# Kernel optimization log

Measured on AMD Instinct MI355X. Metric: run time of the kernel, lower is better.

The kernel has to match this reference:

```python
import jax, jax.numpy as jnp
import numpy as np

N_NODES = 50000
N_EDGES = 800000
DIMX = 64
DIMY = 32
NSMAT = 64
N_MID = 6  # six hidden nsmat->nsmat layers between the input and output projections


def setup_inputs() -> dict:
    key = jax.random.key(0)
    ks = jax.random.split(key, 10)
    node_features = jax.random.normal(ks[0], (N_NODES, DIMX), dtype=jnp.float32)
    edge_index = jax.random.randint(ks[1], (2, N_EDGES), 0, N_NODES, dtype=jnp.int64)
    s_in = 1.0 / np.sqrt(DIMX)
    s_mid = 1.0 / np.sqrt(NSMAT)
    w_in = jax.random.uniform(ks[2], (DIMX, NSMAT), jnp.float32, -s_in, s_in)
    b_in = jax.random.uniform(ks[3], (NSMAT,), jnp.float32, -s_in, s_in)
    w_mid = jax.random.uniform(ks[4], (N_MID, NSMAT, NSMAT), jnp.float32, -s_mid, s_mid)
    b_mid = jax.random.uniform(ks[5], (N_MID, NSMAT), jnp.float32, -s_mid, s_mid)
    w_out = jax.random.uniform(ks[6], (NSMAT, DIMY * DIMX), jnp.float32, -s_mid, s_mid)
    b_out = jax.random.uniform(ks[7], (DIMY * DIMX,), jnp.float32, -s_mid, s_mid)
    return {"node_features": node_features, "edge_index": edge_index,
            "w_in": w_in, "b_in": b_in, "w_mid": w_mid, "b_mid": b_mid,
            "w_out": w_out, "b_out": b_out}


def reference(node_features, edge_index, w_in, b_in, w_mid, b_mid, w_out, b_out):
    # per-node MLP producing a [dimy, dimx] sheaf matrix
    h = jax.nn.relu(node_features @ w_in + b_in)
    for i in range(N_MID):  # fixed small layer count
        h = jax.nn.relu(h @ w_mid[i] + b_mid[i])
    smat = (h @ w_out + b_out).reshape(-1, DIMY, DIMX)  # [N, dimy, dimx]
    # batched matrix-vector transform: q_n = smat_n @ x_n
    q = jnp.einsum('nyx,nx->ny', smat, node_features)  # [N, dimy]
    # LightGCN conv: out_i = sum_{(j->i) in E} q_j / sqrt(deg_j * deg_i)
    row, col = edge_index[0], edge_index[1]
    deg = jax.ops.segment_sum(jnp.ones((N_EDGES,), q.dtype), col, num_segments=N_NODES)
    dinv = jnp.where(deg > 0, jax.lax.rsqrt(jnp.maximum(deg, 1.0)), 0.0)
    norm = dinv[row] * dinv[col]  # [E]
    out = jax.ops.segment_sum(norm[:, None] * q[row], col, num_segments=N_NODES)
    return out
```

## Files before the change

kernel.cpp:

```cpp
#include <hip/hip_runtime.h>
#include <cstddef>

#define N_NODES_C 50000
#define N_NODES_PAD 50048
#define N_EDGES_C 800000
#define CAP 64

typedef _Float16 f16x8 __attribute__((ext_vector_type(8)));
typedef float    f32x4 __attribute__((ext_vector_type(4)));

constexpr int XSTR = 72;
constexpr int MQ_BLOCKS   = 782;
constexpr int DEG_BLOCKS  = 782;
constexpr int FILL_BLOCKS = 782;
constexpr int SCALE_BLOCKS = 391;

__device__ __forceinline__ void gll16(const void* g, void* l) {
    __builtin_amdgcn_global_load_lds(
        (const __attribute__((address_space(1))) void*)g,
        (__attribute__((address_space(3))) void*)l, 16, 0, 0);
}

__global__ void prep_w_kernel(const float* __restrict__ w_in,
                              const float* __restrict__ w_mid,
                              const float* __restrict__ w_out,
                              _Float16* __restrict__ wT,
                              _Float16* __restrict__ W3T)
{
    const int idx = blockIdx.x * 256 + threadIdx.x;
    if (idx < 7 * 4096) {
        const int l = idx >> 12, rem = idx & 4095;
        const int k = rem >> 6, j = rem & 63;
        const float v = (l == 0) ? w_in[k * 64 + j]
                                 : w_mid[(size_t)(l - 1) * 4096 + k * 64 + j];
        wT[(size_t)l * 4096 + j * 64 + k] = (_Float16)v;
    } else {
        const int i2 = idx - 7 * 4096;
        const int k = i2 >> 11, r = i2 & 2047;
        const int c = k >> 3;
        const int pos = ((c ^ (r & 7)) << 3) | (k & 7);
        W3T[(size_t)r * 64 + pos] = (_Float16)w_out[(size_t)k * 2048 + r];
    }
}

__launch_bounds__(256, 4)
__global__ void mega_kernel(const float* __restrict__ xf,
                            const float* __restrict__ b_in,
                            const float* __restrict__ b_mid,
                            const _Float16* __restrict__ wT,
                            const _Float16* __restrict__ W3T,
                            const float* __restrict__ b_out,
                            float* __restrict__ qs,
                            const int* __restrict__ col,
                            int* __restrict__ deg,
                            unsigned char* __restrict__ rank8)
{
    __shared__ _Float16 smem[16896];

    if (blockIdx.x >= MQ_BLOCKS) {
        const int base = (blockIdx.x - MQ_BLOCKS) * 1024 + threadIdx.x;
        #pragma unroll
        for (int u = 0; u < 4; ++u) {
            const int e = base + u * 256;
            if (e < N_EDGES_C)
                rank8[e] = (unsigned char)atomicAdd(&deg[col[e]], 1);
        }
        return;
    }

    const int t    = threadIdx.x;
    const int w    = t >> 6;
    const int lane = t & 63;
    const int quad = lane >> 4;
    const int lrow = lane & 15;
    const int node0 = blockIdx.x * 64 + w * 16;
    _Float16* hb = &smem[w * 16 * XSTR];

    {
        const int n = min(node0 + lrow, N_NODES_C - 1);
        const float4* src4 = (const float4*)(xf + (size_t)n * 64 + quad * 16);
        _Float16 tmp[16];
        #pragma unroll
        for (int i = 0; i < 4; ++i) {
            const float4 v = src4[i];
            tmp[i * 4 + 0] = (_Float16)v.x;
            tmp[i * 4 + 1] = (_Float16)v.y;
            tmp[i * 4 + 2] = (_Float16)v.z;
            tmp[i * 4 + 3] = (_Float16)v.w;
        }
        *(f16x8*)&hb[lrow * XSTR + quad * 16]     = *(f16x8*)&tmp[0];
        *(f16x8*)&hb[lrow * XSTR + quad * 16 + 8] = *(f16x8*)&tmp[8];
    }

    {
        const _Float16* wTl = wT;
        const float* bsrc = b_in;
        for (int l = 0; l < 7; ++l) {
            const f16x8 A0 = *(const f16x8*)&hb[lrow * XSTR + quad * 8];
            const f16x8 A1 = *(const f16x8*)&hb[lrow * XSTR + 32 + quad * 8];
            #pragma unroll
            for (int Nt = 0; Nt < 4; ++Nt) {
                const f16x8 B0 = *(const f16x8*)(wTl + (Nt * 16 + lrow) * 64 + quad * 8);
                const f16x8 B1 = *(const f16x8*)(wTl + (Nt * 16 + lrow) * 64 + 32 + quad * 8);
                const float bias = bsrc[Nt * 16 + lrow];
                f32x4 C = {0.f, 0.f, 0.f, 0.f};
                C = __builtin_amdgcn_mfma_f32_16x16x32_f16(A0, B0, C, 0, 0, 0);
                C = __builtin_amdgcn_mfma_f32_16x16x32_f16(A1, B1, C, 0, 0, 0);
                #pragma unroll
                for (int r = 0; r < 4; ++r) {
                    const float v = fmaxf(C[r] + bias, 0.f);
                    hb[(quad * 4 + r) * XSTR + Nt * 16 + lrow] = (_Float16)v;
                }
            }
            wTl += 4096;
            bsrc = b_mid + (size_t)l * 64;
        }
    }

    const int ra = node0 + lrow;
    const int na = min(ra, N_NODES_C - 1);

    f16x8 Bha[2];
    #pragma unroll
    for (int ks = 0; ks < 2; ++ks)
        Bha[ks] = *(const f16x8*)&hb[lrow * XSTR + ks * 32 + quad * 8];
    float4 xca[4];
    #pragma unroll
    for (int xt = 0; xt < 4; ++xt)
        xca[xt] = *(const float4*)(xf + (size_t)na * 64 + xt * 16 + quad * 4);

    __syncthreads();

    {
        float* lb = (float*)smem;
        const float* gb = b_out + (size_t)(w * 64 + lane) * 4;
        gll16(gb,        lb + w * 256);
        gll16(gb + 1024, lb + 1024 + w * 256);
        #pragma unroll
        for (int s = 0; s < 2; ++s) {
            _Float16* ld = &smem[4608 + s * 4096 + w * 512];
            const _Float16* gs = W3T + (size_t)s * 4096 + (size_t)(w * 64 + lane) * 8;
            gll16(gs,        ld);
            gll16(gs + 2048, ld + 2048);
        }
    }

    const int swz = lrow & 7;
    const int cp0 = ((quad)     ^ swz) * 8;
    const int cp1 = ((4 + quad) ^ swz) * 8;
    const float* lbf = (const float*)smem;

    int rcur = 0;
    for (int y = 0; y < 32; ++y) {
        if (y == 0)      asm volatile("s_waitcnt vmcnt(2)" ::: "memory");
        else if (y == 1) asm volatile("s_waitcnt vmcnt(3)" ::: "memory");
        else             asm volatile("s_waitcnt vmcnt(4)" ::: "memory");
        __builtin_amdgcn_s_barrier();
        __builtin_amdgcn_sched_barrier(0);

        {
            const int ys = (y + 2) & 31;
            const int ri = (rcur == 0) ? 2 : rcur - 1;
            _Float16* ld = &smem[4608 + ri * 4096 + w * 512];
            const _Float16* gs = W3T + (size_t)ys * 4096 + (size_t)(w * 64 + lane) * 8;
            gll16(gs,        ld);
            gll16(gs + 2048, ld + 2048);
        }

        const _Float16* cur = &smem[4608 + rcur * 4096];
        float qa = 0.f;
        #pragma unroll
        for (int xt = 0; xt < 4; ++xt) {
            const _Float16* rp = cur + (xt * 16 + lrow) * 64;
            const f16x8 A0 = *(const f16x8*)(rp + cp0);
            const f16x8 A1 = *(const f16x8*)(rp + cp1);
            f32x4 Ca = {0.f, 0.f, 0.f, 0.f};
            Ca = __builtin_amdgcn_mfma_f32_16x16x32_f16(A0, Bha[0], Ca, 0, 0, 0);
            Ca = __builtin_amdgcn_mfma_f32_16x16x32_f16(A1, Bha[1], Ca, 0, 0, 0);

            const float4 bf = *(const float4*)(lbf + y * 64 + xt * 16 + quad * 4);
            qa += (Ca[0] + bf.x) * xca[xt].x + (Ca[1] + bf.y) * xca[xt].y
                + (Ca[2] + bf.z) * xca[xt].z + (Ca[3] + bf.w) * xca[xt].w;
        }
        qa += __shfl_xor(qa, 16);
        qa += __shfl_xor(qa, 32);

        if (quad == (y >> 3)) {
            qs[(size_t)ra * 32 + y] = qa;
        }

        rcur = (rcur == 2) ? 0 : rcur + 1;
    }
}

__global__ void fill_scale_kernel(const int* __restrict__ row,
                                  const int* __restrict__ col,
                                  const unsigned char* __restrict__ rank8,
                                  const int* __restrict__ deg,
                                  float* __restrict__ qs,
                                  unsigned short* __restrict__ src16)
{
    if (blockIdx.x < FILL_BLOCKS) {
        const int base = blockIdx.x * 1024 + threadIdx.x;
        #pragma unroll
        for (int u = 0; u < 4; ++u) {
            const int e = base + u * 256;
            if (e < N_EDGES_C) {
                const int c = col[e];
                const int r = rank8[e];
                src16[(size_t)c * CAP + r] = (unsigned short)row[e];
            }
        }
    } else {
        const int sb = blockIdx.x - FILL_BLOCKS;
        #pragma unroll
        for (int k = 0; k < 4; ++k) {
            const int idx4 = k * (SCALE_BLOCKS * 256) + sb * 256 + threadIdx.x;
            const int rown = idx4 >> 3;
            const int d = (rown < N_NODES_C) ? deg[rown] : 0;
            const float dv = (d > 0) ? rsqrtf((float)d) : 0.f;
            float4* p = (float4*)qs + idx4;
            float4 v = *p;
            v.x *= dv; v.y *= dv; v.z *= dv; v.w *= dv;
            *p = v;
        }
    }
}

__global__ void gather_kernel(const int* __restrict__ deg,
                              const unsigned short* __restrict__ src16,
                              const float* __restrict__ qs,
                              float* __restrict__ out)
{
    const int t = threadIdx.x;
    const int node = blockIdx.x * 32 + (t >> 3);
    if (node >= N_NODES_C) return;
    const int yq = (t & 7) * 4;
    const int d = deg[node];
    const unsigned short* sp = src16 + (size_t)node * CAP;
    float4 acc = {0.f, 0.f, 0.f, 0.f};
    int s = 0;
    for (; s + 4 <= d; s += 4) {
        const ushort4 r4 = *(const ushort4*)(sp + s);
        const float4 a0 = *(const float4*)(qs + (size_t)r4.x * 32 + yq);
        const float4 a1 = *(const float4*)(qs + (size_t)r4.y * 32 + yq);
        const float4 a2 = *(const float4*)(qs + (size_t)r4.z * 32 + yq);
        const float4 a3 = *(const float4*)(qs + (size_t)r4.w * 32 + yq);
        acc.x += a0.x + a1.x + a2.x + a3.x;
        acc.y += a0.y + a1.y + a2.y + a3.y;
        acc.z += a0.z + a1.z + a2.z + a3.z;
        acc.w += a0.w + a1.w + a2.w + a3.w;
    }
    for (; s < d; ++s) {
        const float4 a = *(const float4*)(qs + (size_t)sp[s] * 32 + yq);
        acc.x += a.x; acc.y += a.y; acc.z += a.z; acc.w += a.w;
    }
    const float dv = (d > 0) ? rsqrtf((float)d) : 0.f;
    float4 r;
    r.x = acc.x * dv; r.y = acc.y * dv; r.z = acc.z * dv; r.w = acc.w * dv;
    *(float4*)(out + (size_t)node * 32 + yq) = r;
}

extern "C" void kernel_launch(void* const* d_in, const int* in_sizes, int n_in,
                              void* d_out, int out_size, void* d_ws, size_t ws_size,
                              hipStream_t stream)
{
    const float* xf    = (const float*)d_in[0];
    const int*   eidx  = (const int*)d_in[1];
    const float* w_in  = (const float*)d_in[2];
    const float* b_in  = (const float*)d_in[3];
    const float* w_mid = (const float*)d_in[4];
    const float* b_mid = (const float*)d_in[5];
    const float* w_out = (const float*)d_in[6];
    const float* b_out = (const float*)d_in[7];
    float* out = (float*)d_out;

    const int* row = eidx;
    const int* col = eidx + N_EDGES_C;

    char* ws = (char*)d_ws;
    float*          qs    = (float*)(ws + 0);
    int*            deg   = (int*)(ws + 6406144);
    _Float16*       wT    = (_Float16*)(ws + 6606336);
    _Float16*       W3T   = (_Float16*)(ws + 6663680);
    unsigned char*  rank8 = (unsigned char*)(ws + 6925824);
    unsigned short* src16 = (unsigned short*)(ws + 7725824);

    hipMemsetAsync(deg, 0, 50048 * sizeof(int), stream);

    prep_w_kernel<<<dim3(624), dim3(256), 0, stream>>>(w_in, w_mid, w_out, wT, W3T);

    mega_kernel<<<dim3(MQ_BLOCKS + DEG_BLOCKS), dim3(256), 0, stream>>>(
        xf, b_in, b_mid, wT, W3T, b_out, qs, col, deg, rank8);

    fill_scale_kernel<<<dim3(FILL_BLOCKS + SCALE_BLOCKS), dim3(256), 0, stream>>>(
        row, col, rank8, deg, qs, src16);

    gather_kernel<<<dim3(1563), dim3(256), 0, stream>>>(deg, src16, qs, out);
}
```

Measured before the change: 168.2 us.

## Fuse CSR fill into degree-count atomics and fold deg memset into prep kernel

The edge-slot write into src16 now happens in the same pass that atomically increments each destination's degree. This removes the rank8 intermediate buffer and the separate fill pass, which re-read col, row and rank8. The hipMemsetAsync of deg is replaced by extra zeroing blocks in prep_w_kernel, which saves one launch. The scale step becomes its own small kernel, and src16 writes are now scattered inside the busier mega kernel.

```diff
diff --git a/kernel.cpp b/kernel.cpp
--- a/kernel.cpp
+++ b/kernel.cpp
@@ -12,7 +12,6 @@
 constexpr int XSTR = 72;
 constexpr int MQ_BLOCKS   = 782;
 constexpr int DEG_BLOCKS  = 782;
-constexpr int FILL_BLOCKS = 782;
 constexpr int SCALE_BLOCKS = 391;
 
 __device__ __forceinline__ void gll16(const void* g, void* l) {
@@ -25,9 +24,19 @@
                               const float* __restrict__ w_mid,
                               const float* __restrict__ w_out,
                               _Float16* __restrict__ wT,
-                              _Float16* __restrict__ W3T)
-{
-    const int idx = blockIdx.x * 256 + threadIdx.x;
+                              _Float16* __restrict__ W3T,
+                              int* __restrict__ deg)
+{
+    const int b = blockIdx.x;
+    if (b >= 624) {
+        const int idx = (b - 624) * 256 + threadIdx.x;
+        if (idx < 50048 / 4) {
+            int4 z = {0, 0, 0, 0};
+            *((int4*)deg + idx) = z;
+        }
+        return;
+    }
+    const int idx = b * 256 + threadIdx.x;
     if (idx < 7 * 4096) {
         const int l = idx >> 12, rem = idx & 4095;
         const int k = rem >> 6, j = rem & 63;
@@ -51,9 +60,10 @@
                             const _Float16* __restrict__ W3T,
                             const float* __restrict__ b_out,
                             float* __restrict__ qs,
+                            const int* __restrict__ row,
                             const int* __restrict__ col,
                             int* __restrict__ deg,
-                            unsigned char* __restrict__ rank8)
+                            unsigned short* __restrict__ src16)
 {
     __shared__ _Float16 smem[16896];
 
@@ -62,8 +72,11 @@
         #pragma unroll
         for (int u = 0; u < 4; ++u) {
             const int e = base + u * 256;
-            if (e < N_EDGES_C)
-                rank8[e] = (unsigned char)atomicAdd(&deg[col[e]], 1);
+            if (e < N_EDGES_C) {
+                const int c = col[e];
+                const int r = atomicAdd(&deg[c], 1);
+                src16[(size_t)c * CAP + r] = (unsigned short)row[e];
+            }
         }
         return;
     }
@@ -193,37 +206,18 @@
     }
 }
 
-__global__ void fill_scale_kernel(const int* __restrict__ row,
-                                  const int* __restrict__ col,
-                                  const unsigned char* __restrict__ rank8,
-                                  const int* __restrict__ deg,
-                                  float* __restrict__ qs,
-                                  unsigned short* __restrict__ src16)
-{
-    if (blockIdx.x < FILL_BLOCKS) {
-        const int base = blockIdx.x * 1024 + threadIdx.x;
-        #pragma unroll
-        for (int u = 0; u < 4; ++u) {
-            const int e = base + u * 256;
-            if (e < N_EDGES_C) {
-                const int c = col[e];
-                const int r = rank8[e];
-                src16[(size_t)c * CAP + r] = (unsigned short)row[e];
-            }
-        }
-    } else {
-        const int sb = blockIdx.x - FILL_BLOCKS;
-        #pragma unroll
-        for (int k = 0; k < 4; ++k) {
-            const int idx4 = k * (SCALE_BLOCKS * 256) + sb * 256 + threadIdx.x;
-            const int rown = idx4 >> 3;
-            const int d = (rown < N_NODES_C) ? deg[rown] : 0;
-            const float dv = (d > 0) ? rsqrtf((float)d) : 0.f;
-            float4* p = (float4*)qs + idx4;
-            float4 v = *p;
-            v.x *= dv; v.y *= dv; v.z *= dv; v.w *= dv;
-            *p = v;
-        }
+__global__ void scale_kernel(const int* __restrict__ deg, float* __restrict__ qs)
+{
+    #pragma unroll
+    for (int k = 0; k < 4; ++k) {
+        const int idx4 = k * (SCALE_BLOCKS * 256) + blockIdx.x * 256 + threadIdx.x;
+        const int rown = idx4 >> 3;
+        const int d = (rown < N_NODES_C) ? deg[rown] : 0;
+        const float dv = (d > 0) ? rsqrtf((float)d) : 0.f;
+        float4* p = (float4*)qs + idx4;
+        float4 v = *p;
+        v.x *= dv; v.y *= dv; v.z *= dv; v.w *= dv;
+        *p = v;
     }
 }
 
@@ -283,18 +277,15 @@
     int*            deg   = (int*)(ws + 6406144);
     _Float16*       wT    = (_Float16*)(ws + 6606336);
     _Float16*       W3T   = (_Float16*)(ws + 6663680);
-    unsigned char*  rank8 = (unsigned char*)(ws + 6925824);
-    unsigned short* src16 = (unsigned short*)(ws + 7725824);
-
-    hipMemsetAsync(deg, 0, 50048 * sizeof(int), stream);
-
-    prep_w_kernel<<<dim3(624), dim3(256), 0, stream>>>(w_in, w_mid, w_out, wT, W3T);
+    unsigned short* src16 = (unsigned short*)(ws + 6925824);
+
+    prep_w_kernel<<<dim3(624 + 49), dim3(256), 0, stream>>>(
+        w_in, w_mid, w_out, wT, W3T, deg);
 
     mega_kernel<<<dim3(MQ_BLOCKS + DEG_BLOCKS), dim3(256), 0, stream>>>(
-        xf, b_in, b_mid, wT, W3T, b_out, qs, col, deg, rank8);
-
-    fill_scale_kernel<<<dim3(FILL_BLOCKS + SCALE_BLOCKS), dim3(256), 0, stream>>>(
-        row, col, rank8, deg, qs, src16);
+        xf, b_in, b_mid, wT, W3T, b_out, qs, row, col, deg, src16);
+
+    scale_kernel<<<dim3(SCALE_BLOCKS), dim3(256), 0, stream>>>(deg, qs);
 
     gather_kernel<<<dim3(1563), dim3(256), 0, stream>>>(deg, src16, qs, out);
 }
```

Result: faster. 161.0 us (-4.2%).
